# Performance work log

Hardware: AMD Instinct MI355X
Metric: run time of the kernel (lower is better)

## Reference

```python
import jax, jax.numpy as jnp
from jax import lax
import numpy as np

EPS = 1e-5
CH = [16, 64, 512]


def _conv(x, w, stride):
    # x: [B,D,H,W,Cin], w: [3,3,3,Cin,Cout], centered kernel (padding 1) like ME kernel_size=3
    return lax.conv_general_dilated(
        x, w, (stride, stride, stride), [(1, 1)] * 3,
        dimension_numbers=('NDHWC', 'DHWIO', 'NDHWC'))


def _bn_elu(x, m, gamma, beta):
    # BatchNorm over ACTIVE sites only (ME stores features only at active coords), training-mode stats.
    mm = m[..., None]
    cnt = jnp.sum(m)
    mean = jnp.sum(x * mm, axis=(0, 1, 2, 3)) / cnt
    var = jnp.sum(jnp.square(x - mean) * mm, axis=(0, 1, 2, 3)) / cnt
    xh = (x - mean) * lax.rsqrt(var + EPS) * gamma + beta
    return jax.nn.elu(xh) * mm


def _pool_mask(m):
    # ME stride-2 conv output coords = unique(in_coord // 2) -> OR over 2x2x2 blocks
    return lax.reduce_window(m, 0.0, lax.max, (1, 2, 2, 2), (1, 2, 2, 2), 'VALID')


def _block(x, m_in, wa, ga, ba, wb, gb, bb):
    m_out = _pool_mask(m_in)
    y = _conv(x, wa, 2) * m_out[..., None]   # strided sparse conv, masked to output coords
    y = _bn_elu(y, m_out, ga, ba)
    y = _conv(y, wb, 1) * m_out[..., None]   # stride-1 conv keeps coordinate set
    y = _bn_elu(y, m_out, gb, bb)
    return y, m_out


def setup_inputs() -> dict:
    key = jax.random.key(0)
    ks = jax.random.split(key, 16)
    B, G = 4, 128
    x = jax.random.normal(ks[0], (B, G, G, G, 1), dtype=jnp.float32)
    mask = jax.random.randint(ks[1], (B, G, G, G), 0, 2, dtype=jnp.int32)

    def kconv(k, cin, cout):
        std = np.sqrt(2.0 / (27 * cout))  # kaiming_normal_ fan_out, relu
        return jax.random.normal(k, (3, 3, 3, cin, cout), dtype=jnp.float32) * std

    inp = {'x': x, 'mask': mask,
           'w1a': kconv(ks[2], 1, CH[0]),  'g1a': jnp.ones((CH[0],)), 'b1a': jnp.zeros((CH[0],)),
           'w1b': kconv(ks[3], CH[0], CH[0]), 'g1b': jnp.ones((CH[0],)), 'b1b': jnp.zeros((CH[0],)),
           'w2a': kconv(ks[4], CH[0], CH[1]), 'g2a': jnp.ones((CH[1],)), 'b2a': jnp.zeros((CH[1],)),
           'w2b': kconv(ks[5], CH[1], CH[1]), 'g2b': jnp.ones((CH[1],)), 'b2b': jnp.zeros((CH[1],)),
           'w3a': kconv(ks[6], CH[1], CH[2]), 'g3a': jnp.ones((CH[2],)), 'b3a': jnp.zeros((CH[2],)),
           'w3b': kconv(ks[7], CH[2], CH[2]), 'g3b': jnp.ones((CH[2],)), 'b3b': jnp.zeros((CH[2],)),
           'wm': jax.random.normal(ks[8], (CH[2], CH[2]), dtype=jnp.float32) / np.sqrt(CH[2]),
           'bm': jnp.zeros((CH[2],)),
           'wv': jax.random.normal(ks[9], (CH[2], CH[2]), dtype=jnp.float32) / np.sqrt(CH[2]),
           'bv': jnp.zeros((CH[2],))}
    return inp


def reference(x, mask, w1a, g1a, b1a, w1b, g1b, b1b,
              w2a, g2a, b2a, w2b, g2b, b2b,
              w3a, g3a, b3a, w3b, g3b, b3b,
              wm, bm, wv, bv):
    m0 = mask.astype(jnp.float32)
    h = x * m0[..., None]  # features exist only at active coordinates
    h, m1 = _block(h, m0, w1a, g1a, b1a, w1b, g1b, b1b)
    h, m2 = _block(h, m1, w2a, g2a, b2a, w2b, g2b, b2b)
    h, m3 = _block(h, m2, w3a, g3a, b3a, w3b, g3b, b3b)
    # MinkowskiGlobalPooling: per-batch mean over active sites -> [B, 512]
    denom = jnp.sum(m3, axis=(1, 2, 3), keepdims=False)[:, None]
    pooled = jnp.sum(h * m3[..., None], axis=(1, 2, 3)) / denom
    mean = pooled @ wm + bm
    log_var = pooled @ wv + bv
    return mean, log_var
```

## Files before the change

kernel.cpp:

```cpp
#include <hip/hip_runtime.h>
#include <cstddef>


#define EPSV 1e-5f

typedef _Float16 f16x4 __attribute__((ext_vector_type(4)));
typedef _Float16 f16x8 __attribute__((ext_vector_type(8)));
typedef float f32x4 __attribute__((ext_vector_type(4)));

template <int KC> struct FragSel;
template <> struct FragSel<32> { using T = f16x8; };
template <> struct FragSel<16> { using T = f16x4; };

__device__ __forceinline__ f32x4 mfma16(f16x8 a, f16x8 b, f32x4 c) {
    return __builtin_amdgcn_mfma_f32_16x16x32_f16(a, b, c, 0, 0, 0);
}
__device__ __forceinline__ f32x4 mfma16(f16x4 a, f16x4 b, f32x4 c) {
    return __builtin_amdgcn_mfma_f32_16x16x16f16(a, b, c, 0, 0, 0);
}

__device__ __forceinline__ void gld16(const void* g, void* l) {
    __builtin_amdgcn_global_load_lds(
        (const __attribute__((address_space(1))) unsigned int*)g,
        (__attribute__((address_space(3))) unsigned int*)l, 16, 0, 0);
}

__device__ __forceinline__ int swz(int b) { return b ^ ((b >> 3) & 0x70); }

__global__ __launch_bounds__(256) void pool23_kernel(const float* __restrict__ m1,
                                                     float* __restrict__ m2,
                                                     float* __restrict__ m3,
                                                     float* __restrict__ cnt2,
                                                     float* __restrict__ cnt3,
                                                     float* __restrict__ cnt3b) {
    int bid = blockIdx.x;
    int tw4 = bid & 3, th4 = (bid >> 2) & 3, td8 = (bid >> 4) & 7, b = bid >> 7;
    int tid = threadIdx.x;
    int lw = tid & 7, lh = (tid >> 3) & 7, ld = tid >> 6;
    int wo = tw4 * 8 + lw, ho = th4 * 8 + lh, dd = td8 * 4 + ld;
    float mx = 0.f;
#pragma unroll
    for (int dz = 0; dz < 2; ++dz)
#pragma unroll
        for (int hy = 0; hy < 2; ++hy)
#pragma unroll
            for (int wx = 0; wx < 2; ++wx) {
                size_t idx = ((size_t)((b * 64 + 2 * dd + dz) * 64 + 2 * ho + hy)) * 64
                             + 2 * wo + wx;
                mx = fmaxf(mx, m1[idx]);
            }
    m2[((size_t)((b * 32 + dd) * 32 + ho)) * 32 + wo] = mx;

    __shared__ float red[256];
    __shared__ float red3[32];
    red[tid] = mx;
    __syncthreads();
    if (((tid & 1) | ((tid >> 3) & 1) | ((tid >> 6) & 1)) == 0) {
        float v = red[tid];
        v = fmaxf(v, red[tid ^ 1]);
        v = fmaxf(v, red[tid ^ 8]);
        v = fmaxf(v, red[tid ^ 9]);
        v = fmaxf(v, red[tid ^ 64]);
        v = fmaxf(v, red[tid ^ 65]);
        v = fmaxf(v, red[tid ^ 72]);
        v = fmaxf(v, red[tid ^ 73]);
        int w3 = wo >> 1, h3 = ho >> 1, d3 = dd >> 1;
        m3[((size_t)((b * 16 + d3) * 16 + h3)) * 16 + w3] = v;
        int i32 = (lw >> 1) + 4 * (lh >> 1) + 16 * (ld >> 1);
        red3[i32] = v;
    }
    __syncthreads();
    for (int st = 128; st > 0; st >>= 1) {
        if (tid < st) red[tid] += red[tid + st];
        __syncthreads();
    }
    if (tid < 16) red3[tid] += red3[tid + 16];
    __syncthreads();
    if (tid < 8) red3[tid] += red3[tid + 8];
    __syncthreads();
    if (tid == 0) {
        float s3 = red3[0] + red3[1] + red3[2] + red3[3] + red3[4] + red3[5] + red3[6] + red3[7];
        atomicAdd(cnt2, red[0]);
        atomicAdd(cnt3, s3);
        atomicAdd(&cnt3b[b], s3);
    }
}

__global__ __launch_bounds__(256) void wtrans_all(
    const float* __restrict__ w1b, const float* __restrict__ w2a,
    const float* __restrict__ w2b, const float* __restrict__ w3a,
    const float* __restrict__ w3b,
    _Float16* __restrict__ o1b, _Float16* __restrict__ o2a,
    _Float16* __restrict__ o2b, _Float16* __restrict__ o3a,
    _Float16* __restrict__ o3b) {
    __shared__ float tile[32][33];
    int bid = blockIdx.x;
    const float* W; _Float16* O; int CIN, COUT, rel, TCO;
    if (bid < 27)        { W = w1b; O = o1b; CIN = 16;  COUT = 16;  rel = bid;        TCO = 1; }
    else if (bid < 81)   { W = w2a; O = o2a; CIN = 16;  COUT = 64;  rel = bid - 27;   TCO = 2; }
    else if (bid < 189)  { W = w2b; O = o2b; CIN = 64;  COUT = 64;  rel = bid - 81;   TCO = 2; }
    else if (bid < 1053) { W = w3a; O = o3a; CIN = 64;  COUT = 512; rel = bid - 189;  TCO = 16; }
    else                 { W = w3b; O = o3b; CIN = 512; COUT = 512; rel = bid - 1053; TCO = 16; }
    int TCI = (CIN + 31) >> 5;
    int per_t = TCI * TCO;
    int t = rel / per_t;
    int rr = rel - t * per_t;
    int tci = rr / TCO, tco = rr - tci * TCO;
    int ci0 = tci * 32, co0 = tco * 32;
    int tid = threadIdx.x;
    int c32 = tid & 31, r8 = tid >> 5;
#pragma unroll
    for (int j = 0; j < 4; ++j) {
        int ci = ci0 + j * 8 + r8, co = co0 + c32;
        if (ci < CIN && co < COUT)
            tile[j * 8 + r8][c32] = W[((size_t)t * CIN + ci) * COUT + co];
    }
    __syncthreads();
#pragma unroll
    for (int j = 0; j < 4; ++j) {
        int co = co0 + j * 8 + r8, ci = ci0 + c32;
        if (co < COUT && ci < CIN)
            O[((size_t)t * COUT + co) * CIN + ci] = (_Float16)tile[c32][j * 8 + r8];
    }
}

__global__ __launch_bounds__(256) void conv1a_kernel(const float* __restrict__ x,
                                                     const int* __restrict__ mask,
                                                     const float* __restrict__ w,
                                                     float* __restrict__ m1,
                                                     _Float16* __restrict__ out,
                                                     float* __restrict__ stats,
                                                     float* __restrict__ cnt_total) {
    int voxel = blockIdx.x * 256 + threadIdx.x;
    int wo = voxel & 63, ho = (voxel >> 6) & 63, dd = (voxel >> 12) & 63, b = voxel >> 18;

    int any = 0;
#pragma unroll
    for (int dz = 0; dz < 2; ++dz)
#pragma unroll
        for (int hy = 0; hy < 2; ++hy)
#pragma unroll
            for (int wx = 0; wx < 2; ++wx) {
                size_t idx = ((size_t)((b * 128 + 2 * dd + dz) * 128 + 2 * ho + hy)) * 128
                             + 2 * wo + wx;
                any |= mask[idx];
            }
    float mv = any ? 1.f : 0.f;
    m1[voxel] = mv;

    float acc[16];
#pragma unroll
    for (int i = 0; i < 16; ++i) acc[i] = 0.f;
    for (int kd = 0; kd < 3; ++kd) {
        int id = 2 * dd + kd - 1;
        if ((unsigned)id >= 128u) continue;
        for (int kh = 0; kh < 3; ++kh) {
            int ih = 2 * ho + kh - 1;
            if ((unsigned)ih >= 128u) continue;
            for (int kw = 0; kw < 3; ++kw) {
                int iw = 2 * wo + kw - 1;
                if ((unsigned)iw >= 128u) continue;
                size_t idx = ((size_t)((b * 128 + id) * 128 + ih)) * 128 + iw;
                float xv = x[idx] * (float)mask[idx];
                const float* wp = w + ((kd * 3 + kh) * 3 + kw) * 16;
#pragma unroll
                for (int co = 0; co < 16; ++co) acc[co] = fmaf(xv, wp[co], acc[co]);
            }
        }
    }
    _Float16* op = out + (size_t)voxel * 16;
    __shared__ float red[256 * 32];
    __shared__ float redm[256];
#pragma unroll
    for (int co = 0; co < 16; ++co) {
        float v = acc[co] * mv;
        op[co] = (_Float16)v;
        red[threadIdx.x * 32 + co] = v;
        red[threadIdx.x * 32 + 16 + co] = v * v;
    }
    redm[threadIdx.x] = mv;
    __syncthreads();
    for (int st = 128; st > 0; st >>= 1) {
        if (threadIdx.x < st) {
#pragma unroll
            for (int k = 0; k < 32; ++k)
                red[threadIdx.x * 32 + k] += red[(threadIdx.x + st) * 32 + k];
            redm[threadIdx.x] += redm[threadIdx.x + st];
        }
        __syncthreads();
    }
    if (threadIdx.x < 32) {
        float* sb = stats + (blockIdx.x & 7) * 32;
        atomicAdd(&sb[threadIdx.x], red[threadIdx.x]);
    }
    if (threadIdx.x == 32) atomicAdd(cnt_total, redm[0]);
}

template <int CIN, int COUT, int NTILE, int STRIDE, int NIN, int NOUT,
          int TW, int LTW, int TH, int LTH, int TD, int WM, int MINW, int TAPG,
          bool STATS, bool FUSEIN>
__global__ __launch_bounds__(256, MINW) void conv_mfma(const _Float16* __restrict__ in,
                                                       const _Float16* __restrict__ wt,
                                                       const float* __restrict__ mout,
                                                       _Float16* __restrict__ out,
                                                       const _Float16* __restrict__ zbuf,
                                                       float* __restrict__ stats,
                                                       const float* __restrict__ min_,
                                                       const float* __restrict__ statsi,
                                                       const float* __restrict__ cnti,
                                                       const float* __restrict__ gin,
                                                       const float* __restrict__ bin) {
    constexpr int M = TW * TH * TD;
    constexpr int KC = (CIN >= 32) ? 32 : 16;
    constexpr int KB = KC * 2;
    constexpr int LKB = (KC >= 32) ? 6 : 5;
    constexpr int HW_ = (TW - 1) * STRIDE + 3;
    constexpr int HH_ = (TH - 1) * STRIDE + 3;
    constexpr int HD_ = (TD - 1) * STRIDE + 3;
    constexpr int HV = HW_ * HH_ * HD_;
    constexpr int LPV = KB / 16;
    constexpr int VPI = 64 / LPV;
    constexpr int NIH = (HV + VPI - 1) / VPI;
    constexpr int HVP = NIH * VPI;
    constexpr int WN = 4 / WM;
    constexpr int WMT = M / WM;
    constexpr int WNT = NTILE / WN;
    constexpr int NAF = WMT / 16;
    constexpr int NBF = WNT / 16;
    constexpr int NBLK = COUT / NTILE;
    constexpr int NTW = NOUT / TW, NTH = NOUT / TH, NTD = NOUT / TD;
    constexpr int NUMM = 4 * NTW * NTH * NTD;
    constexpr int BI = (NTILE * KB + 1023) / 1024;
    constexpr int NG = 27 / TAPG;
    constexpr int BTAP = NTILE * KB;
    static_assert(!FUSEIN || CIN == KC, "FUSEIN requires single K-chunk");

    using Frag = typename FragSel<KC>::T;

    __shared__ _Float16 halo[HVP * KC];
    __shared__ _Float16 bbuf[2 * TAPG * NTILE * KC];
    __shared__ float cfs[FUSEIN ? 2 * CIN : 2];

    int cpx = gridDim.x >> 3;
    int bid = (blockIdx.x & 7) * cpx + (blockIdx.x >> 3);

    int nblk = (NBLK > 1) ? bid / NUMM : 0;
    int mblk = (NBLK > 1) ? bid % NUMM : bid;
    int tw = mblk % NTW;
    int th = (mblk / NTW) % NTH;
    int td = (mblk / (NTW * NTH)) % NTD;
    int b = mblk / (NTW * NTH * NTD);
    int d0 = td * TD * STRIDE - 1, h0 = th * TH * STRIDE - 1, w0 = tw * TW * STRIDE - 1;

    int tid = threadIdx.x;
    int wv = tid >> 6, lane = tid & 63, m16 = lane & 15, quad = lane >> 4;
    int wm_ = wv % WM, wn_ = wv / WM;
    int qb = quad * (KB / 4);

    const int nissue = ((wv < BI) ? 1 : 0) + ((wv + 4 < BI) ? 1 : 0);

    if constexpr (FUSEIN) {
        float cn = *cnti;
        for (int c = tid; c < CIN; c += 256) {
            float s = 0.f, q = 0.f;
#pragma unroll
            for (int k = 0; k < 8; ++k) {
                s += statsi[k * 2 * CIN + c];
                q += statsi[k * 2 * CIN + CIN + c];
            }
            float mean = s / cn;
            float var = q / cn - mean * mean;
            float sc = rsqrtf(var + EPSV) * gin[c];
            cfs[c] = sc;
            cfs[CIN + c] = bin[c] - mean * sc;
        }
    }

    int abase_b[NAF];
#pragma unroll
    for (int r = 0; r < NAF; ++r) {
        int vloc = wm_ * WMT + r * 16 + m16;
        int vw = vloc & (TW - 1), vh = (vloc >> LTW) & (TH - 1), vd = vloc >> (LTW + LTH);
        int avox = ((vd * STRIDE) * HH_ + vh * STRIDE) * HW_ + vw * STRIDE;
        abase_b[r] = avox * KB + qb;
    }
    int bofsw[NBF];
#pragma unroll
    for (int f = 0; f < NBF; ++f)
        bofsw[f] = swz((wn_ * WNT + f * 16 + m16) * KB + qb);

    int bsrc[2];
    bool bok[2];
#pragma unroll
    for (int k = 0; k < 2; ++k) {
        int i = wv + 4 * k;
        int S = i * 1024 + lane * 16;
        int Bq = swz(S);
        int row = Bq >> LKB;
        int cb = Bq & (KB - 1);
        bsrc[k] = row * CIN + (cb >> 1);
        bok[k] = (i < BI) && ((BTAP % 1024 == 0) || (row < NTILE));
    }

    f32x4 acc[NAF][NBF];
#pragma unroll
    for (int r = 0; r < NAF; ++r)
#pragma unroll
        for (int f = 0; f < NBF; ++f) acc[r][f] = (f32x4){0.f, 0.f, 0.f, 0.f};

    auto stage_halo = [&](int c0) {
        for (int i = wv; i < NIH; i += 4) {
            int S = i * 1024 + lane * 16;
            int Bq = swz(S);
            int hv = Bq >> LKB;
            int cb = Bq & (KB - 1);
            int hw = hv % HW_;
            int t2 = hv / HW_;
            int hh = t2 % HH_;
            int hd = t2 / HH_;
            int d = d0 + hd, h = h0 + hh, w = w0 + hw;
            bool ok = (hv < HV) && ((unsigned)d < (unsigned)NIN) &&
                      ((unsigned)h < (unsigned)NIN) && ((unsigned)w < (unsigned)NIN);
            if constexpr (FUSEIN) {
                f16x8 o = (f16x8){0, 0, 0, 0, 0, 0, 0, 0};
                if (ok) {
                    size_t gvox = ((size_t)(((b * NIN + d) * NIN + h) * NIN + w));
                    f16x8 xv = *(const f16x8*)(in + gvox * CIN + (cb >> 1));
                    float mv = min_[gvox];
                    int cc = cb >> 1;
#pragma unroll
                    for (int k = 0; k < 8; ++k) {
                        float xh = (float)xv[k] * cfs[cc + k] + cfs[CIN + cc + k];
                        float e = xh > 0.f ? xh : expm1f(xh);
                        o[k] = (_Float16)(e * mv);
                    }
                }
                *(f16x8*)((char*)halo + S) = o;
            } else {
                const _Float16* g =
                    ok ? in + ((size_t)(((b * NIN + d) * NIN + h) * NIN + w)) * CIN + c0
                             + (cb >> 1)
                       : zbuf;
                gld16(g, (char*)halo + i * 1024);
            }
        }
    };

    auto stage_B = [&](int tap, int jslot, int c0) {
        const _Float16* wb = wt + (size_t)tap * (COUT * CIN) + (size_t)nblk * NTILE * CIN + c0;
#pragma unroll
        for (int k = 0; k < 2; ++k) {
            if (bok[k])
                gld16(wb + bsrc[k], (char*)bbuf + (size_t)jslot * BTAP + (wv + 4 * k) * 1024);
        }
    };

    for (int c0 = 0; c0 < CIN; c0 += KC) {
        __syncthreads();
        stage_halo(c0);
        if constexpr (FUSEIN) asm volatile("s_waitcnt lgkmcnt(0)" ::: "memory");
#pragma unroll
        for (int j = 0; j < TAPG; ++j) stage_B(j, j, c0);

        for (int g = 0; g < NG; ++g) {
            asm volatile("s_barrier" ::: "memory");
            if (g + 1 < NG) {
                int tb2 = (g + 1) * TAPG;
                int js = ((g + 1) & 1) * TAPG;
#pragma unroll
                for (int j = 0; j < TAPG; ++j) stage_B(tb2 + j, js + j, c0);
                if (nissue == 2)
                    asm volatile("s_waitcnt vmcnt(%0)" :: "i"(2 * TAPG) : "memory");
                else if (nissue == 1)
                    asm volatile("s_waitcnt vmcnt(%0)" :: "i"(TAPG) : "memory");
                else
                    asm volatile("s_waitcnt vmcnt(0)" ::: "memory");
            } else {
                asm volatile("s_waitcnt vmcnt(0)" ::: "memory");
            }
            asm volatile("s_barrier" ::: "memory");

            int tb = g * TAPG;
            int kd = tb / 9, rr = tb - kd * 9, kh = rr / 3, kw = rr - kh * 3;
            int tvb = ((kd * HH_ + kh) * HW_ + kw) * KB;
            const char* bp = (const char*)bbuf + (size_t)((g & 1) * TAPG) * BTAP;
            __builtin_amdgcn_s_setprio(1);
#pragma unroll
            for (int j = 0; j < TAPG; ++j) {
                Frag a[NAF], bb[NBF];
#pragma unroll
                for (int r = 0; r < NAF; ++r)
                    a[r] = *(const Frag*)((const char*)halo + swz(abase_b[r] + tvb + j * KB));
#pragma unroll
                for (int f = 0; f < NBF; ++f)
                    bb[f] = *(const Frag*)(bp + (size_t)j * BTAP + bofsw[f]);
#pragma unroll
                for (int r = 0; r < NAF; ++r)
#pragma unroll
                    for (int f = 0; f < NBF; ++f) acc[r][f] = mfma16(a[r], bb[f], acc[r][f]);
            }
            __builtin_amdgcn_s_setprio(0);
        }
    }

    int n0 = nblk * NTILE + wn_ * WNT + m16;
    float sv[NBF], qv[NBF];
    if constexpr (STATS) {
#pragma unroll
        for (int f = 0; f < NBF; ++f) { sv[f] = 0.f; qv[f] = 0.f; }
    }
#pragma unroll
    for (int r = 0; r < NAF; ++r) {
#pragma unroll
        for (int j = 0; j < 4; ++j) {
            int vloc = wm_ * WMT + r * 16 + quad * 4 + j;
            int vw = vloc & (TW - 1), vh = (vloc >> LTW) & (TH - 1), vd = vloc >> (LTW + LTH);
            int od = td * TD + vd, oh = th * TH + vh, ow = tw * TW + vw;
            size_t gvox = ((size_t)((b * NOUT + od) * NOUT + oh)) * NOUT + ow;
            float mv = mout[gvox];
            _Float16* op = out + gvox * COUT + n0;
#pragma unroll
            for (int f = 0; f < NBF; ++f) {
                float val = acc[r][f][j] * mv;
                op[f * 16] = (_Float16)val;
                if constexpr (STATS) { sv[f] += val; qv[f] += val * val; }
            }
        }
    }
    if constexpr (STATS) {
        float* sb = stats + (blockIdx.x & 7) * (2 * COUT);
#pragma unroll
        for (int f = 0; f < NBF; ++f) {
            float s = sv[f], q = qv[f];
            s += __shfl_xor(s, 16);
            s += __shfl_xor(s, 32);
            q += __shfl_xor(q, 16);
            q += __shfl_xor(q, 32);
            if (lane < 16) {
                int c = n0 + f * 16;
                atomicAdd(&sb[c], s);
                atomicAdd(&sb[COUT + c], q);
            }
        }
    }
}

template <int C, int LOGC>
__global__ __launch_bounds__(256) void bn_apply2(_Float16* __restrict__ x,
                                                 const float* __restrict__ m,
                                                 const float* __restrict__ stats,
                                                 const float* __restrict__ cntp,
                                                 const float* __restrict__ gamma,
                                                 const float* __restrict__ beta, long n) {
    __shared__ float cf[2 * C];
    float cn = *cntp;
    for (int c = threadIdx.x; c < C; c += 256) {
        float s = 0.f, q = 0.f;
#pragma unroll
        for (int k = 0; k < 8; ++k) {
            s += stats[k * 2 * C + c];
            q += stats[k * 2 * C + C + c];
        }
        float mean = s / cn;
        float var = q / cn - mean * mean;
        float sc = rsqrtf(var + EPSV) * gamma[c];
        cf[c] = sc;
        cf[C + c] = beta[c] - mean * sc;
    }
    __syncthreads();
    long stride = (long)gridDim.x * 2048;
    for (long i8 = ((long)blockIdx.x * 256 + threadIdx.x) * 8; i8 < n; i8 += stride) {
        int c = (int)(i8 & (C - 1));
        long v = i8 >> LOGC;
        f16x8 xv = *(const f16x8*)(x + i8);
        float mv = m[v];
        f16x8 o;
#pragma unroll
        for (int k = 0; k < 8; ++k) {
            float xh = (float)xv[k] * cf[c + k] + cf[C + c + k];
            float e = xh > 0.f ? xh : expm1f(xh);
            o[k] = (_Float16)(e * mv);
        }
        *(f16x8*)(x + i8) = o;
    }
}

__global__ __launch_bounds__(256) void gpool_kernel(const _Float16* __restrict__ h,
                                                    const float* __restrict__ m3,
                                                    const float* __restrict__ stats,
                                                    const float* __restrict__ cntp,
                                                    const float* __restrict__ gamma,
                                                    const float* __restrict__ beta,
                                                    float* __restrict__ pooled) {
    __shared__ float cf[1024];
    float cn = *cntp;
    for (int c = threadIdx.x; c < 512; c += 256) {
        float s = 0.f, q = 0.f;
#pragma unroll
        for (int k = 0; k < 8; ++k) {
            s += stats[k * 1024 + c];
            q += stats[k * 1024 + 512 + c];
        }
        float mean = s / cn;
        float var = q / cn - mean * mean;
        float sc = rsqrtf(var + EPSV) * gamma[c];
        cf[c] = sc;
        cf[512 + c] = beta[c] - mean * sc;
    }
    __syncthreads();
    int b = blockIdx.x >> 6, seg = blockIdx.x & 63;
    int ch = (threadIdx.x & 63) * 8;
    int v0 = threadIdx.x >> 6;
    float scl[8], shf[8];
#pragma unroll
    for (int k = 0; k < 8; ++k) {
        scl[k] = cf[ch + k];
        shf[k] = cf[512 + ch + k];
    }
    float s[8];
#pragma unroll
    for (int k = 0; k < 8; ++k) s[k] = 0.f;
    for (int v = v0; v < 64; v += 4) {
        int vox = b * 4096 + seg * 64 + v;
        float mv = m3[vox];
        f16x8 xv = *(const f16x8*)(h + (size_t)vox * 512 + ch);
#pragma unroll
        for (int k = 0; k < 8; ++k) {
            float xh = (float)xv[k] * scl[k] + shf[k];
            float e = xh > 0.f ? xh : expm1f(xh);
            s[k] += e * mv;
        }
    }
#pragma unroll
    for (int k = 0; k < 8; ++k) atomicAdd(&pooled[b * 512 + ch + k], s[k]);
}

__global__ __launch_bounds__(256) void head_kernel(const float* __restrict__ pooled,
                                                   const float* __restrict__ cntb,
                                                   const float* __restrict__ wm,
                                                   const float* __restrict__ bm,
                                                   const float* __restrict__ wv,
                                                   const float* __restrict__ bv,
                                                   float* __restrict__ out) {
    int t = blockIdx.x * 256 + threadIdx.x;
    int which = t >> 11;
    int b = (t >> 9) & 3;
    int j = t & 511;
    const float* W = which ? wv : wm;
    float bias = which ? bv[j] : bm[j];
    const float* p = pooled + b * 512;
    float s = 0.f;
    for (int c = 0; c < 512; ++c) s = fmaf(p[c], W[c * 512 + j], s);
    out[t] = s / cntb[b] + bias;
}

extern "C" void kernel_launch(void* const* d_in, const int* in_sizes, int n_in,
                              void* d_out, int out_size, void* d_ws, size_t ws_size,
                              hipStream_t stream) {
    const float* x   = (const float*)d_in[0];
    const int* mask  = (const int*)d_in[1];
    const float* w1a = (const float*)d_in[2];
    const float* g1a = (const float*)d_in[3];
    const float* b1a = (const float*)d_in[4];
    const float* w1b = (const float*)d_in[5];
    const float* g1b = (const float*)d_in[6];
    const float* b1b = (const float*)d_in[7];
    const float* w2a = (const float*)d_in[8];
    const float* g2a = (const float*)d_in[9];
    const float* b2a = (const float*)d_in[10];
    const float* w2b = (const float*)d_in[11];
    const float* g2b = (const float*)d_in[12];
    const float* b2b = (const float*)d_in[13];
    const float* w3a = (const float*)d_in[14];
    const float* g3a = (const float*)d_in[15];
    const float* b3a = (const float*)d_in[16];
    const float* w3b = (const float*)d_in[17];
    const float* g3b = (const float*)d_in[18];
    const float* b3b = (const float*)d_in[19];
    const float* wm  = (const float*)d_in[20];
    const float* bm  = (const float*)d_in[21];
    const float* wv  = (const float*)d_in[22];
    const float* bv  = (const float*)d_in[23];
    float* out = (float*)d_out;

    char* ws = (char*)d_ws;
    _Float16* A  = (_Float16*)(ws + 0);
    _Float16* Bb = (_Float16*)(ws + 33554432);
    _Float16* w1bh = (_Float16*)(ws + 67108864);
    _Float16* w2ah = (_Float16*)(ws + 67125248);
    _Float16* w2bh = (_Float16*)(ws + 67182592);
    _Float16* w3ah = (_Float16*)(ws + 67403776);
    _Float16* w3bh = (_Float16*)(ws + 69173248);
    float* m1 = (float*)(ws + 83329024);
    float* m2 = (float*)(ws + 87523328);
    float* m3 = (float*)(ws + 88047616);
    float* counts = (float*)(ws + 88113152);
    float* stats  = (float*)(ws + 88113216);
    float* pooled = (float*)(ws + 88309824);
    _Float16* zbuf = (_Float16*)(ws + 88318016);

    float* sL0 = stats;
    float* sL1 = stats + 1 * 8192;
    float* sL2 = stats + 2 * 8192;
    float* sL3 = stats + 3 * 8192;
    float* sL4 = stats + 4 * 8192;
    float* sL5 = stats + 5 * 8192;

    _Float16* h1a = A;
    _Float16* h1b = Bb;
    _Float16* h2a = A;
    _Float16* h2b = Bb;
    _Float16* h3a = A;
    _Float16* h3b = Bb;

    hipMemsetAsync(counts, 0, 64 + 196608 + 8192 + 256, stream);

    wtrans_all<<<7965, 256, 0, stream>>>(w1b, w2a, w2b, w3a, w3b,
                                         w1bh, w2ah, w2bh, w3ah, w3bh);

    conv1a_kernel<<<4096, 256, 0, stream>>>(x, mask, w1a, m1, h1a, sL0, counts + 0);
    pool23_kernel<<<512, 256, 0, stream>>>(m1, m2, m3, counts + 1, counts + 2, counts + 4);

    conv_mfma<16, 16, 16, 1, 64, 64, 8, 3, 8, 3, 8, 4, 4, 3, true, true>
        <<<2048, 256, 0, stream>>>(h1a, w1bh, m1, h1b, zbuf, sL1,
                                   m1, sL0, counts + 0, g1a, b1a);

    conv_mfma<16, 64, 64, 2, 64, 32, 8, 3, 4, 2, 4, 2, 2, 3, true, true>
        <<<1024, 256, 0, stream>>>(h1b, w2ah, m2, h2a, zbuf, sL2,
                                   m1, sL1, counts + 0, g1b, b1b);
    bn_apply2<64, 6><<<1024, 256, 0, stream>>>(h2a, m2, sL2, counts + 1, g2a, b2a, 8388608L);

    conv_mfma<64, 64, 64, 1, 32, 32, 8, 3, 8, 3, 4, 2, 2, 3, true, false>
        <<<512, 256, 0, stream>>>(h2a, w2bh, m2, h2b, zbuf, sL3,
                                  nullptr, nullptr, nullptr, nullptr, nullptr);
    bn_apply2<64, 6><<<1024, 256, 0, stream>>>(h2b, m2, sL3, counts + 1, g2b, b2b, 8388608L);

    conv_mfma<64, 512, 128, 2, 32, 16, 4, 2, 4, 2, 4, 2, 2, 1, true, false>
        <<<1024, 256, 0, stream>>>(h2b, w3ah, m3, h3a, zbuf, sL4,
                                   nullptr, nullptr, nullptr, nullptr, nullptr);
    bn_apply2<512, 9><<<512, 256, 0, stream>>>(h3a, m3, sL4, counts + 2, g3a, b3a, 8388608L);

    conv_mfma<512, 512, 128, 1, 16, 16, 8, 3, 4, 2, 4, 2, 2, 3, true, false>
        <<<512, 256, 0, stream>>>(h3a, w3bh, m3, h3b, zbuf, sL5,
                                  nullptr, nullptr, nullptr, nullptr, nullptr);

    gpool_kernel<<<256, 256, 0, stream>>>(h3b, m3, sL5, counts + 2, g3b, b3b, pooled);
    head_kernel<<<16, 256, 0, stream>>>(pooled, counts + 4, wm, bm, wv, bv, out);
}
```

Baseline: 840.2 us.

## Merge prep kernels, fuse BN-ELU into conv2b input, simplify pipeline waits

Merges the weight-transpose and conv1a kernels into a single launch, and makes the conv2b stage apply the BN+ELU of conv2a while loading its input halo (FUSEIN with a channel offset c0), which removes one bn_apply2 pass over memory. The ELU now uses __expf-1 instead of expm1f, trading some precision near zero for speed. The hand-written vmcnt waits and raw s_barriers in the tap-group loop are replaced by a plain __syncthreads, which may lose the overlap between loading weight tiles and running MFMAs, and could race if the global-to-LDS loads have not completed. The static_assert limiting FUSEIN to a single K-chunk is removed and the halo indexing is extended to handle multiple chunks.

```diff
diff --git a/kernel.cpp b/kernel.cpp
--- a/kernel.cpp
+++ b/kernel.cpp
@@ -26,6 +26,8 @@
 }
 
 __device__ __forceinline__ int swz(int b) { return b ^ ((b >> 3) & 0x70); }
+
+__device__ __forceinline__ float elu_(float x) { return x > 0.f ? x : __expf(x) - 1.f; }
 
 __global__ __launch_bounds__(256) void pool23_kernel(const float* __restrict__ m1,
                                                      float* __restrict__ m2,
@@ -86,51 +88,49 @@
     }
 }
 
-__global__ __launch_bounds__(256) void wtrans_all(
+__global__ __launch_bounds__(256) void prep_kernel(
+    const float* __restrict__ x, const int* __restrict__ mask,
+    const float* __restrict__ w1a, float* __restrict__ m1,
+    _Float16* __restrict__ out, float* __restrict__ stats,
+    float* __restrict__ cnt_total,
     const float* __restrict__ w1b, const float* __restrict__ w2a,
     const float* __restrict__ w2b, const float* __restrict__ w3a,
     const float* __restrict__ w3b,
     _Float16* __restrict__ o1b, _Float16* __restrict__ o2a,
     _Float16* __restrict__ o2b, _Float16* __restrict__ o3a,
     _Float16* __restrict__ o3b) {
-    __shared__ float tile[32][33];
-    int bid = blockIdx.x;
-    const float* W; _Float16* O; int CIN, COUT, rel, TCO;
-    if (bid < 27)        { W = w1b; O = o1b; CIN = 16;  COUT = 16;  rel = bid;        TCO = 1; }
-    else if (bid < 81)   { W = w2a; O = o2a; CIN = 16;  COUT = 64;  rel = bid - 27;   TCO = 2; }
-    else if (bid < 189)  { W = w2b; O = o2b; CIN = 64;  COUT = 64;  rel = bid - 81;   TCO = 2; }
-    else if (bid < 1053) { W = w3a; O = o3a; CIN = 64;  COUT = 512; rel = bid - 189;  TCO = 16; }
-    else                 { W = w3b; O = o3b; CIN = 512; COUT = 512; rel = bid - 1053; TCO = 16; }
-    int TCI = (CIN + 31) >> 5;
-    int per_t = TCI * TCO;
-    int t = rel / per_t;
-    int rr = rel - t * per_t;
-    int tci = rr / TCO, tco = rr - tci * TCO;
-    int ci0 = tci * 32, co0 = tco * 32;
-    int tid = threadIdx.x;
-    int c32 = tid & 31, r8 = tid >> 5;
-#pragma unroll
-    for (int j = 0; j < 4; ++j) {
-        int ci = ci0 + j * 8 + r8, co = co0 + c32;
-        if (ci < CIN && co < COUT)
-            tile[j * 8 + r8][c32] = W[((size_t)t * CIN + ci) * COUT + co];
-    }
-    __syncthreads();
-#pragma unroll
-    for (int j = 0; j < 4; ++j) {
-        int co = co0 + j * 8 + r8, ci = ci0 + c32;
-        if (co < COUT && ci < CIN)
-            O[((size_t)t * COUT + co) * CIN + ci] = (_Float16)tile[c32][j * 8 + r8];
-    }
-}
-
-__global__ __launch_bounds__(256) void conv1a_kernel(const float* __restrict__ x,
-                                                     const int* __restrict__ mask,
-                                                     const float* __restrict__ w,
-                                                     float* __restrict__ m1,
-                                                     _Float16* __restrict__ out,
-                                                     float* __restrict__ stats,
-                                                     float* __restrict__ cnt_total) {
+    if (blockIdx.x >= 4096) {
+        __shared__ float tile[32][33];
+        int bid = blockIdx.x - 4096;
+        const float* W; _Float16* O; int CIN, COUT, rel, TCO;
+        if (bid < 27)        { W = w1b; O = o1b; CIN = 16;  COUT = 16;  rel = bid;        TCO = 1; }
+        else if (bid < 81)   { W = w2a; O = o2a; CIN = 16;  COUT = 64;  rel = bid - 27;   TCO = 2; }
+        else if (bid < 189)  { W = w2b; O = o2b; CIN = 64;  COUT = 64;  rel = bid - 81;   TCO = 2; }
+        else if (bid < 1053) { W = w3a; O = o3a; CIN = 64;  COUT = 512; rel = bid - 189;  TCO = 16; }
+        else                 { W = w3b; O = o3b; CIN = 512; COUT = 512; rel = bid - 1053; TCO = 16; }
+        int TCI = (CIN + 31) >> 5;
+        int per_t = TCI * TCO;
+        int t = rel / per_t;
+        int rr = rel - t * per_t;
+        int tci = rr / TCO, tco = rr - tci * TCO;
+        int ci0 = tci * 32, co0 = tco * 32;
+        int tid = threadIdx.x;
+        int c32 = tid & 31, r8 = tid >> 5;
+#pragma unroll
+        for (int j = 0; j < 4; ++j) {
+            int ci = ci0 + j * 8 + r8, co = co0 + c32;
+            if (ci < CIN && co < COUT)
+                tile[j * 8 + r8][c32] = W[((size_t)t * CIN + ci) * COUT + co];
+        }
+        __syncthreads();
+#pragma unroll
+        for (int j = 0; j < 4; ++j) {
+            int co = co0 + j * 8 + r8, ci = ci0 + c32;
+            if (co < COUT && ci < CIN)
+                O[((size_t)t * COUT + co) * CIN + ci] = (_Float16)tile[c32][j * 8 + r8];
+        }
+        return;
+    }
     int voxel = blockIdx.x * 256 + threadIdx.x;
     int wo = voxel & 63, ho = (voxel >> 6) & 63, dd = (voxel >> 12) & 63, b = voxel >> 18;
 
@@ -162,7 +162,7 @@
                 if ((unsigned)iw >= 128u) continue;
                 size_t idx = ((size_t)((b * 128 + id) * 128 + ih)) * 128 + iw;
                 float xv = x[idx] * (float)mask[idx];
-                const float* wp = w + ((kd * 3 + kh) * 3 + kw) * 16;
+                const float* wp = w1a + ((kd * 3 + kh) * 3 + kw) * 16;
 #pragma unroll
                 for (int co = 0; co < 16; ++co) acc[co] = fmaf(xv, wp[co], acc[co]);
             }
@@ -233,7 +233,6 @@
     constexpr int BI = (NTILE * KB + 1023) / 1024;
     constexpr int NG = 27 / TAPG;
     constexpr int BTAP = NTILE * KB;
-    static_assert(!FUSEIN || CIN == KC, "FUSEIN requires single K-chunk");
 
     using Frag = typename FragSel<KC>::T;
 
@@ -256,8 +255,6 @@
     int wv = tid >> 6, lane = tid & 63, m16 = lane & 15, quad = lane >> 4;
     int wm_ = wv % WM, wn_ = wv / WM;
     int qb = quad * (KB / 4);
-
-    const int nissue = ((wv < BI) ? 1 : 0) + ((wv + 4 < BI) ? 1 : 0);
 
     if constexpr (FUSEIN) {
         float cn = *cnti;
@@ -325,14 +322,13 @@
                 f16x8 o = (f16x8){0, 0, 0, 0, 0, 0, 0, 0};
                 if (ok) {
                     size_t gvox = ((size_t)(((b * NIN + d) * NIN + h) * NIN + w));
-                    f16x8 xv = *(const f16x8*)(in + gvox * CIN + (cb >> 1));
+                    f16x8 xv = *(const f16x8*)(in + gvox * CIN + c0 + (cb >> 1));
                     float mv = min_[gvox];
-                    int cc = cb >> 1;
+                    int cc = c0 + (cb >> 1);
 #pragma unroll
                     for (int k = 0; k < 8; ++k) {
                         float xh = (float)xv[k] * cfs[cc + k] + cfs[CIN + cc + k];
-                        float e = xh > 0.f ? xh : expm1f(xh);
-                        o[k] = (_Float16)(e * mv);
+                        o[k] = (_Float16)(elu_(xh) * mv);
                     }
                 }
                 *(f16x8*)((char*)halo + S) = o;
@@ -358,28 +354,17 @@
     for (int c0 = 0; c0 < CIN; c0 += KC) {
         __syncthreads();
         stage_halo(c0);
-        if constexpr (FUSEIN) asm volatile("s_waitcnt lgkmcnt(0)" ::: "memory");
 #pragma unroll
         for (int j = 0; j < TAPG; ++j) stage_B(j, j, c0);
 
         for (int g = 0; g < NG; ++g) {
-            asm volatile("s_barrier" ::: "memory");
+            __syncthreads();
             if (g + 1 < NG) {
                 int tb2 = (g + 1) * TAPG;
                 int js = ((g + 1) & 1) * TAPG;
 #pragma unroll
                 for (int j = 0; j < TAPG; ++j) stage_B(tb2 + j, js + j, c0);
-                if (nissue == 2)
-                    asm volatile("s_waitcnt vmcnt(%0)" :: "i"(2 * TAPG) : "memory");
-                else if (nissue == 1)
-                    asm volatile("s_waitcnt vmcnt(%0)" :: "i"(TAPG) : "memory");
-                else
-                    asm volatile("s_waitcnt vmcnt(0)" ::: "memory");
-            } else {
-                asm volatile("s_waitcnt vmcnt(0)" ::: "memory");
-            }
-            asm volatile("s_barrier" ::: "memory");
-
+            }
             int tb = g * TAPG;
             int kd = tb / 9, rr = tb - kd * 9, kh = rr / 3, kw = rr - kh * 3;
             int tvb = ((kd * HH_ + kh) * HW_ + kw) * KB;
@@ -478,8 +463,7 @@
 #pragma unroll
         for (int k = 0; k < 8; ++k) {
             float xh = (float)xv[k] * cf[c + k] + cf[C + c + k];
-            float e = xh > 0.f ? xh : expm1f(xh);
-            o[k] = (_Float16)(e * mv);
+            o[k] = (_Float16)(elu_(xh) * mv);
         }
         *(f16x8*)(x + i8) = o;
     }
@@ -527,8 +511,7 @@
 #pragma unroll
         for (int k = 0; k < 8; ++k) {
             float xh = (float)xv[k] * scl[k] + shf[k];
-            float e = xh > 0.f ? xh : expm1f(xh);
-            s[k] += e * mv;
+            s[k] += elu_(xh) * mv;
         }
     }
 #pragma unroll
@@ -615,10 +598,9 @@
 
     hipMemsetAsync(counts, 0, 64 + 196608 + 8192 + 256, stream);
 
-    wtrans_all<<<7965, 256, 0, stream>>>(w1b, w2a, w2b, w3a, w3b,
-                                         w1bh, w2ah, w2bh, w3ah, w3bh);
-
-    conv1a_kernel<<<4096, 256, 0, stream>>>(x, mask, w1a, m1, h1a, sL0, counts + 0);
+    prep_kernel<<<12061, 256, 0, stream>>>(x, mask, w1a, m1, h1a, sL0, counts + 0,
+                                           w1b, w2a, w2b, w3a, w3b,
+                                           w1bh, w2ah, w2bh, w3ah, w3bh);
     pool23_kernel<<<512, 256, 0, stream>>>(m1, m2, m3, counts + 1, counts + 2, counts + 4);
 
     conv_mfma<16, 16, 16, 1, 64, 64, 8, 3, 8, 3, 8, 4, 4, 3, true, true>
@@ -628,11 +610,10 @@
     conv_mfma<16, 64, 64, 2, 64, 32, 8, 3, 4, 2, 4, 2, 2, 3, true, true>
         <<<1024, 256, 0, stream>>>(h1b, w2ah, m2, h2a, zbuf, sL2,
                                    m1, sL1, counts + 0, g1b, b1b);
-    bn_apply2<64, 6><<<1024, 256, 0, stream>>>(h2a, m2, sL2, counts + 1, g2a, b2a, 8388608L);
-
-    conv_mfma<64, 64, 64, 1, 32, 32, 8, 3, 8, 3, 4, 2, 2, 3, true, false>
+
+    conv_mfma<64, 64, 64, 1, 32, 32, 8, 3, 8, 3, 4, 2, 2, 3, true, true>
         <<<512, 256, 0, stream>>>(h2a, w2bh, m2, h2b, zbuf, sL3,
-                                  nullptr, nullptr, nullptr, nullptr, nullptr);
+                                  m2, sL2, counts + 1, g2a, b2a);
     bn_apply2<64, 6><<<1024, 256, 0, stream>>>(h2b, m2, sL3, counts + 1, g2b, b2b, 8388608L);
 
     conv_mfma<64, 512, 128, 2, 32, 16, 4, 2, 4, 2, 4, 2, 2, 1, true, false>
```

Result: faster. 815.8 us (median of 2 runs) (-2.9%).
